# Kernel optimization log

Measured on AMD Instinct MI355X. Metric: run time of the kernel, lower is better.

## Reference

```python
import jax, jax.numpy as jnp
import numpy as np

N = 50000      # nodes
E = 800000     # edges (before self-loops)
IN_DIM = 128
OUT_DIM = 64   # per-head channels C (concat=False)
HEADS = 4
NEG_SLOPE = 0.2


def setup_inputs() -> dict:
    key = jax.random.key(0)
    ks = jax.random.split(key, 10)
    x = jax.random.normal(ks[0], (N, IN_DIM), dtype=jnp.float32)
    edge_index = jax.random.randint(ks[1], (2, E), 0, N, dtype=jnp.int32)
    # GAT parameters
    W = jax.random.normal(ks[2], (IN_DIM, HEADS * OUT_DIM), dtype=jnp.float32) * 0.05
    att_src = jax.random.normal(ks[3], (HEADS, OUT_DIM), dtype=jnp.float32) * 0.05
    att_dst = jax.random.normal(ks[4], (HEADS, OUT_DIM), dtype=jnp.float32) * 0.05
    bias = jnp.zeros((OUT_DIM,), dtype=jnp.float32)
    # LayerNorm + PReLU parameters
    gamma = jnp.ones((OUT_DIM,), dtype=jnp.float32)
    beta = jnp.zeros((OUT_DIM,), dtype=jnp.float32)
    prelu_w = jnp.full((1,), 0.25, dtype=jnp.float32)
    return {"x": x, "edge_index": edge_index, "W": W, "att_src": att_src,
            "att_dst": att_dst, "bias": bias, "gamma": gamma, "beta": beta,
            "prelu_w": prelu_w}


def reference(x, edge_index, W, att_src, att_dst, bias, gamma, beta, prelu_w):
    n = x.shape[0]
    # PyG GATConv default add_self_loops=True
    loops = jnp.arange(n, dtype=edge_index.dtype)
    src = jnp.concatenate([edge_index[0], loops])  # message sources j
    dst = jnp.concatenate([edge_index[1], loops])  # message targets i

    # linear projection into heads: [N, H, C]
    h = (x @ W).reshape(n, HEADS, OUT_DIM)
    a_src = jnp.einsum('nhc,hc->nh', h, att_src)  # [N, H]
    a_dst = jnp.einsum('nhc,hc->nh', h, att_dst)  # [N, H]

    # per-edge attention logits, leaky relu
    alpha = a_src[src] + a_dst[dst]                       # [E', H]
    alpha = jnp.where(alpha >= 0, alpha, NEG_SLOPE * alpha)

    # segment softmax over incoming edges of each destination node
    amax = jax.ops.segment_max(alpha, dst, num_segments=n)   # [N, H]
    e = jnp.exp(alpha - amax[dst])
    denom = jax.ops.segment_sum(e, dst, num_segments=n)      # [N, H]
    w = e / denom[dst]                                       # [E', H]

    # weighted scatter-aggregate of messages
    msg = h[src] * w[:, :, None]                             # [E', H, C]
    out = jax.ops.segment_sum(msg, dst, num_segments=n)      # [N, H, C]

    # concat=False -> mean over heads, then bias
    out = out.mean(axis=1) + bias                            # [N, C]

    # LayerNorm
    mu = out.mean(axis=-1, keepdims=True)
    var = out.var(axis=-1, keepdims=True)
    out = (out - mu) * jax.lax.rsqrt(var + 1e-5) * gamma + beta

    # PReLU (single shared weight)
    return jnp.where(out >= 0, out, prelu_w[0] * out)
```

## Files before the change

kernel.cpp:

```cpp
#include <hip/hip_runtime.h>

#define HEADS 4
#define CDIM  64
#define INDIM 128
#define NEG   0.2f
#define CAP     256
#define FASTCAP 252
#define NPB     256

typedef __attribute__((ext_vector_type(8))) short short8;
typedef __attribute__((ext_vector_type(4))) float f32x4;
typedef _Float16 half2_t __attribute__((ext_vector_type(2)));

__device__ __forceinline__ float wave_sum(float v) {
#pragma unroll
    for (int o = 32; o > 0; o >>= 1) v += __shfl_xor(v, o, 64);
    return v;
}
__device__ __forceinline__ int wave_sum_i(int v) {
#pragma unroll
    for (int o = 32; o > 0; o >>= 1) v += __shfl_xor(v, o, 64);
    return v;
}

__device__ __forceinline__ unsigned short f2bf(float f) {
    unsigned u = __float_as_uint(f);
    u = (u + 0x7FFFu + ((u >> 16) & 1u)) >> 16;
    return (unsigned short)u;
}

__device__ __forceinline__ unsigned pk_f16(float a, float b) {
    auto h = __builtin_amdgcn_cvt_pkrtz(a, b);
    return __builtin_bit_cast(unsigned, h);
}
__device__ __forceinline__ half2_t as_h2(unsigned u) {
    return __builtin_bit_cast(half2_t, u);
}

#if __has_builtin(__builtin_amdgcn_fdot2)
__device__ __forceinline__ float fdot2(unsigned a, unsigned b, float c) {
    return __builtin_amdgcn_fdot2(as_h2(a), as_h2(b), c, false);
}
#else
__device__ __forceinline__ float fdot2(unsigned a, unsigned b, float c) {
    half2_t ha = as_h2(a), hb = as_h2(b);
    return c + (float)ha.x * (float)hb.x + (float)ha.y * (float)hb.y;
}
#endif

__device__ __forceinline__ float lrelu(float a) { return a >= 0.f ? a : NEG * a; }

__global__ __launch_bounds__(256) void k_prep(const float* __restrict__ W,
    const float* __restrict__ att_src, const float* __restrict__ att_dst,
    unsigned short* __restrict__ Waug)
{
    const int wv = threadIdx.x >> 6, lane = threadIdx.x & 63;
    const int c = blockIdx.x * 4 + wv;
    if (c >= 272) return;
#pragma unroll
    for (int kk = 0; kk < 2; ++kk) {
        int k = lane + kk * 64;
        float val;
        if (c < 256) {
            val = W[k * 256 + c];
        } else if (c < 260) {
            int q = c - 256; float s = 0.f;
            for (int j = 0; j < 64; ++j) s += W[k * 256 + q * 64 + j] * att_src[q * 64 + j];
            val = s;
        } else if (c < 264) {
            int q = c - 260; float s = 0.f;
            for (int j = 0; j < 64; ++j) s += W[k * 256 + q * 64 + j] * att_dst[q * 64 + j];
            val = s;
        } else {
            val = 0.f;
        }
        Waug[c * 128 + k] = f2bf(val);
    }
}

__global__ __launch_bounds__(512) void gemm_mfma(
    const float* __restrict__ x, const unsigned short* __restrict__ Waug,
    uint2* __restrict__ hp, float* __restrict__ a_src, float* __restrict__ a_dst,
    int N)
{
    extern __shared__ char smem[];
    const int t = threadIdx.x;

    const uint4* srcw = (const uint4*)Waug;
    for (int i = t; i < 272 * 16; i += 512) {
        int col = i >> 4, kc = i & 15;
        int off = col * 256 + ((kc * 16) ^ ((col & 7) << 4));
        *(uint4*)(smem + off) = srcw[i];
    }
    __syncthreads();

    const int lane = t & 63, wv = t >> 6;
    const int l = lane & 15, g = lane >> 4;
    const int rowbase = blockIdx.x * 128 + wv * 16;

    int anode = rowbase + l; if (anode >= N) anode = N - 1;
    const float4* xrow = (const float4*)(x + (size_t)anode * INDIM);

    short8 af[4];
#pragma unroll
    for (int ks = 0; ks < 4; ++ks) {
        float4 x0 = xrow[ks * 8 + g * 2];
        float4 x1 = xrow[ks * 8 + g * 2 + 1];
        short8 a;
        a[0] = (short)f2bf(x0.x); a[1] = (short)f2bf(x0.y);
        a[2] = (short)f2bf(x0.z); a[3] = (short)f2bf(x0.w);
        a[4] = (short)f2bf(x1.x); a[5] = (short)f2bf(x1.y);
        a[6] = (short)f2bf(x1.z); a[7] = (short)f2bf(x1.w);
        af[ks] = a;
    }

    f32x4 acc[17];
    const f32x4 zero = {0.f, 0.f, 0.f, 0.f};
#pragma unroll
    for (int tt = 0; tt < 17; ++tt) acc[tt] = zero;

    const int base_b = l * 256;
#pragma unroll
    for (int ks = 0; ks < 4; ++ks) {
        const int koff = (ks * 64 + g * 16) ^ ((l & 7) << 4);
#pragma unroll
        for (int tt = 0; tt < 17; ++tt) {
            short8 bf = *(const short8*)(smem + tt * 4096 + base_b + koff);
            acc[tt] = __builtin_amdgcn_mfma_f32_16x16x32_bf16(af[ks], bf, acc[tt], 0, 0, 0);
        }
    }

#pragma unroll
    for (int j = 0; j < 4; ++j) {
        int node = rowbase + g * 4 + j;
        if (node < N) {
#pragma unroll
            for (int u = 0; u < 4; ++u) {
                int ch = l + 16 * u;
                hp[(size_t)node * CDIM + ch] = make_uint2(
                    pk_f16(acc[u][j],     acc[4 + u][j]),
                    pk_f16(acc[8 + u][j], acc[12 + u][j]));
            }
            if (l < 4)      a_src[node * 4 + l]       = acc[16][j];
            else if (l < 8) a_dst[node * 4 + (l - 4)] = acc[16][j];
        }
    }
}


__global__ __launch_bounds__(256) void k_count(const int* __restrict__ ei,
    int E, int EPB, int NBUK, int* __restrict__ counts)
{
    __shared__ int hist[256];
    const int t = threadIdx.x, blk = blockIdx.x;
    if (t < NBUK) hist[t] = 0;
    __syncthreads();
    const int e0 = blk * EPB;
    for (int j = t; j < EPB; j += 256) {
        int e = e0 + j;
        if (e < E) atomicAdd(&hist[ei[E + e] >> 8], 1);
    }
    __syncthreads();
    if (t < NBUK) counts[t * NPB + blk] = hist[t];
}

__global__ __launch_bounds__(256) void k_scan1(const int* __restrict__ arr,
    int* __restrict__ bsum, int n)
{
    const int t = threadIdx.x, lane = t & 63, wv = t >> 6;
    int gid = blockIdx.x * 256 + t;
    int v = (gid < n) ? arr[gid] : 0;
    v = wave_sum_i(v);
    __shared__ int ws[4];
    if (lane == 0) ws[wv] = v;
    __syncthreads();
    if (t == 0) bsum[blockIdx.x] = ws[0] + ws[1] + ws[2] + ws[3];
}

__global__ __launch_bounds__(1024) void k_scan2(int* __restrict__ bsum, int NB)
{
    __shared__ int lds[1024];
    const int t = threadIdx.x;
    int v = (t < NB) ? bsum[t] : 0;
    lds[t] = v;
    __syncthreads();
    for (int o = 1; o < 1024; o <<= 1) {
        int u = (t >= o) ? lds[t - o] : 0;
        __syncthreads();
        lds[t] += u;
        __syncthreads();
    }
    if (t < NB) bsum[t] = lds[t] - v;
}

__global__ __launch_bounds__(256) void k_scanip(int* __restrict__ arr,
    const int* __restrict__ bsum, int n)
{
    const int t = threadIdx.x, lane = t & 63, wv = t >> 6;
    int gid = blockIdx.x * 256 + t;
    int v = (gid < n) ? arr[gid] : 0;
    int inc = v;
#pragma unroll
    for (int o = 1; o < 64; o <<= 1) {
        int u = __shfl_up(inc, o, 64);
        if (lane >= o) inc += u;
    }
    __shared__ int wtot[4];
    if (lane == 63) wtot[wv] = inc;
    __syncthreads();
    int wpre = 0;
    for (int w = 0; w < wv; ++w) wpre += wtot[w];
    int ex = inc - v + wpre + bsum[blockIdx.x];
    if (gid < n) arr[gid] = ex;
}

__global__ __launch_bounds__(256) void k_part(const int* __restrict__ ei,
    int E, int EPB, int NBUK, const int* __restrict__ counts,
    uint2* __restrict__ srt)
{
    __shared__ int cb[256];
    const int t = threadIdx.x, blk = blockIdx.x;
    if (t < NBUK) cb[t] = counts[t * NPB + blk];
    __syncthreads();
    const int e0 = blk * EPB;
    for (int j = t; j < EPB; j += 256) {
        int e = e0 + j;
        if (e < E) {
            int s = ei[e], d = ei[E + e];
            int pos = atomicAdd(&cb[d >> 8], 1);
            srt[pos] = make_uint2((unsigned)s, (unsigned)d);
        }
    }
}

__global__ __launch_bounds__(256) void k_bcsr(const uint2* __restrict__ srt,
    const int* __restrict__ counts, int E, int N, int NBUK,
    int* __restrict__ deg, int* __restrict__ off, int* __restrict__ csr)
{
    __shared__ int h[256];
    __shared__ int cur[256];
    __shared__ int wt[4];
    const int t = threadIdx.x, b = blockIdx.x;
    const int bb0 = counts[b * NPB];
    const int bb1 = (b + 1 < NBUK) ? counts[(b + 1) * NPB] : E;
    const int ne = bb1 - bb0;

    h[t] = 0;
    __syncthreads();
    for (int j = t; j < ne; j += 256) atomicAdd(&h[srt[bb0 + j].y & 255], 1);
    __syncthreads();

    int v = h[t];
    const int lane = t & 63, wv = t >> 6;
    int inc = v;
#pragma unroll
    for (int o = 1; o < 64; o <<= 1) {
        int u = __shfl_up(inc, o, 64);
        if (lane >= o) inc += u;
    }
    if (lane == 63) wt[wv] = inc;
    __syncthreads();
    int wpre = 0;
    for (int w = 0; w < wv; ++w) wpre += wt[w];
    int ex = inc - v + wpre;

    int node = (b << 8) + t;
    if (node < N) { deg[node] = v; off[node] = bb0 + ex; }
    cur[t] = bb0 + ex;
    __syncthreads();

    for (int j = t; j < ne; j += 256) {
        uint2 u = srt[bb0 + j];
        int pos = atomicAdd(&cur[u.y & 255], 1);
        csr[pos] = (int)u.x;
    }
}

__global__ __launch_bounds__(256) void aggr_fused(
    const int* __restrict__ off, const int* __restrict__ deg,
    const int* __restrict__ csr_src,
    const float4* __restrict__ a_src4, const float4* __restrict__ a_dst4,
    const uint2* __restrict__ hp,
    const float* __restrict__ bias, const float* __restrict__ gamma,
    const float* __restrict__ beta, const float* __restrict__ prelu,
    float* __restrict__ out, int N)
{
    __shared__ uint4 slot[4][CAP];
    const int wv   = threadIdx.x >> 6;
    const int lane = threadIdx.x & 63;
    const int wid  = (int)(blockIdx.x * 4u + wv);
    if (wid >= N) return;
    const int d = wid;
    uint4* sl = slot[wv];

    const float4 ad = a_dst4[d];
    const int deg_d = deg[d];
    const int beg   = off[d];
    const int nv    = deg_d < FASTCAP ? deg_d : FASTCAP;
    const int nv4   = (nv + 3) & ~3;

    float dl0 = 0.f, dl1 = 0.f, dl2 = 0.f, dl3 = 0.f;
    for (int base = 0; base < deg_d; base += 64) {
        int j = base + lane;
        bool valid = j < deg_d;
        int sv = valid ? csr_src[beg + j] : 0;
        float4 as = a_src4[sv];
        float e0 = valid ? __expf(lrelu(as.x + ad.x)) : 0.f;
        float e1 = valid ? __expf(lrelu(as.y + ad.y)) : 0.f;
        float e2 = valid ? __expf(lrelu(as.z + ad.z)) : 0.f;
        float e3 = valid ? __expf(lrelu(as.w + ad.w)) : 0.f;
        dl0 += e0; dl1 += e1; dl2 += e2; dl3 += e3;
        if (j < CAP) sl[j] = make_uint4(pk_f16(e0, e1), pk_f16(e2, e3), (unsigned)sv, 0u);
    }

    float4 asd = a_src4[d];
    float es0 = __expf(lrelu(asd.x + ad.x));
    float es1 = __expf(lrelu(asd.y + ad.y));
    float es2 = __expf(lrelu(asd.z + ad.z));
    float es3 = __expf(lrelu(asd.w + ad.w));

    float r0 = __builtin_amdgcn_rcpf(wave_sum(dl0) + es0);
    float r1 = __builtin_amdgcn_rcpf(wave_sum(dl1) + es1);
    float r2 = __builtin_amdgcn_rcpf(wave_sum(dl2) + es2);
    float r3 = __builtin_amdgcn_rcpf(wave_sum(dl3) + es3);

    for (int base = 0; base < nv4; base += 64) {
        int j = base + lane;
        if (j < nv) {
            uint2 ev = *(const uint2*)&sl[j];
            half2_t e01 = as_h2(ev.x), e23 = as_h2(ev.y);
            *(uint2*)&sl[j] = make_uint2(
                pk_f16((float)e01.x * r0, (float)e01.y * r1),
                pk_f16((float)e23.x * r2, (float)e23.y * r3));
        } else if (j < nv4) {
            sl[j] = make_uint4(0u, 0u, 0u, 0u);
        }
    }
    __builtin_amdgcn_wave_barrier();

    uint2 hd = hp[(size_t)d * CDIM + lane];
    unsigned pw01 = pk_f16(es0 * r0, es1 * r1);
    unsigned pw23 = pk_f16(es2 * r2, es3 * r3);
    float acc01 = fdot2(pw01, hd.x, 0.f);
    float acc23 = fdot2(pw23, hd.y, 0.f);

    if (nv4 >= 8) {
        uint4 c0 = sl[0], c1 = sl[1], c2 = sl[2], c3 = sl[3];
        uint2 h0 = hp[(size_t)c0.z * CDIM + lane];
        uint2 h1 = hp[(size_t)c1.z * CDIM + lane];
        uint2 h2 = hp[(size_t)c2.z * CDIM + lane];
        uint2 h3 = hp[(size_t)c3.z * CDIM + lane];
        int j = 0;
        for (; j + 7 < nv4; j += 4) {
            uint4 n0 = sl[j + 4], n1 = sl[j + 5], n2 = sl[j + 6], n3 = sl[j + 7];
            uint2 g0 = hp[(size_t)n0.z * CDIM + lane];
            uint2 g1 = hp[(size_t)n1.z * CDIM + lane];
            uint2 g2 = hp[(size_t)n2.z * CDIM + lane];
            uint2 g3 = hp[(size_t)n3.z * CDIM + lane];
            acc01 = fdot2(c0.x, h0.x, acc01); acc23 = fdot2(c0.y, h0.y, acc23);
            acc01 = fdot2(c1.x, h1.x, acc01); acc23 = fdot2(c1.y, h1.y, acc23);
            acc01 = fdot2(c2.x, h2.x, acc01); acc23 = fdot2(c2.y, h2.y, acc23);
            acc01 = fdot2(c3.x, h3.x, acc01); acc23 = fdot2(c3.y, h3.y, acc23);
            c0 = n0; c1 = n1; c2 = n2; c3 = n3;
            h0 = g0; h1 = g1; h2 = g2; h3 = g3;
        }
        acc01 = fdot2(c0.x, h0.x, acc01); acc23 = fdot2(c0.y, h0.y, acc23);
        acc01 = fdot2(c1.x, h1.x, acc01); acc23 = fdot2(c1.y, h1.y, acc23);
        acc01 = fdot2(c2.x, h2.x, acc01); acc23 = fdot2(c2.y, h2.y, acc23);
        acc01 = fdot2(c3.x, h3.x, acc01); acc23 = fdot2(c3.y, h3.y, acc23);
    } else if (nv4 == 4) {
        uint4 c0 = sl[0], c1 = sl[1], c2 = sl[2], c3 = sl[3];
        uint2 h0 = hp[(size_t)c0.z * CDIM + lane];
        uint2 h1 = hp[(size_t)c1.z * CDIM + lane];
        uint2 h2 = hp[(size_t)c2.z * CDIM + lane];
        uint2 h3 = hp[(size_t)c3.z * CDIM + lane];
        acc01 = fdot2(c0.x, h0.x, acc01); acc23 = fdot2(c0.y, h0.y, acc23);
        acc01 = fdot2(c1.x, h1.x, acc01); acc23 = fdot2(c1.y, h1.y, acc23);
        acc01 = fdot2(c2.x, h2.x, acc01); acc23 = fdot2(c2.y, h2.y, acc23);
        acc01 = fdot2(c3.x, h3.x, acc01); acc23 = fdot2(c3.y, h3.y, acc23);
    }

    for (int base = FASTCAP; base < deg_d; base += 64) {
        int jj = base + lane;
        bool valid = jj < deg_d;
        int sv = valid ? csr_src[beg + jj] : 0;
        float4 as = a_src4[sv];
        float e0 = valid ? __expf(lrelu(as.x + ad.x)) : 0.f;
        float e1 = valid ? __expf(lrelu(as.y + ad.y)) : 0.f;
        float e2 = valid ? __expf(lrelu(as.z + ad.z)) : 0.f;
        float e3 = valid ? __expf(lrelu(as.w + ad.w)) : 0.f;
        sl[lane] = make_uint4(pk_f16(e0 * r0, e1 * r1), pk_f16(e2 * r2, e3 * r3),
                              (unsigned)sv, 0u);
        __builtin_amdgcn_wave_barrier();
        int nav = deg_d - base; if (nav > 64) nav = 64;
        for (int q = 0; q < nav; ++q) {
            uint4 t0 = sl[q];
            uint2 h0 = hp[(size_t)t0.z * CDIM + lane];
            acc01 = fdot2(t0.x, h0.x, acc01);
            acc23 = fdot2(t0.y, h0.y, acc23);
        }
        __builtin_amdgcn_wave_barrier();
    }

    float v = 0.25f * (acc01 + acc23) + bias[lane];
    float mu  = wave_sum(v) * (1.f / 64.f);
    float df  = v - mu;
    float var = wave_sum(df * df) * (1.f / 64.f);
    float rs  = rsqrtf(var + 1e-5f);
    float o   = df * rs * gamma[lane] + beta[lane];
    float pw  = prelu[0];
    o = o >= 0.f ? o : pw * o;
    out[(size_t)d * CDIM + lane] = o;
}

extern "C" void kernel_launch(void* const* d_in, const int* in_sizes, int n_in,
                              void* d_out, int out_size, void* d_ws, size_t ws_size,
                              hipStream_t stream)
{
    const float* x       = (const float*)d_in[0];
    const int*   ei      = (const int*)  d_in[1];
    const float* W       = (const float*)d_in[2];
    const float* att_src = (const float*)d_in[3];
    const float* att_dst = (const float*)d_in[4];
    const float* bias    = (const float*)d_in[5];
    const float* gamma   = (const float*)d_in[6];
    const float* beta    = (const float*)d_in[7];
    const float* prelu   = (const float*)d_in[8];

    const int N = in_sizes[0] / INDIM;
    const int E = in_sizes[1] / 2;
    float* out = (float*)d_out;

    const int NBUK = (N + 255) >> 8;
    const int EPB  = (E + NPB - 1) / NPB;
    const int NCNT = NBUK * NPB;

    uint2* hp     = (uint2*)d_ws;
    float* a_src  = (float*)(hp + (size_t)N * CDIM);
    float* a_dst  = a_src + (size_t)N * HEADS;
    int*   deg    = (int*)(a_dst + (size_t)N * HEADS);
    int*   off    = deg + N;
    int*   counts = off + N;
    int*   bsum   = counts + NCNT;
    uint2* srt    = (uint2*)(bsum + 1024);
    int*   csr    = (int*)(srt + E);
    unsigned short* Waug = (unsigned short*)(csr + E);

    k_prep<<<68, 256, 0, stream>>>(W, att_src, att_dst, Waug);

    k_count<<<NPB, 256, 0, stream>>>(ei, E, EPB, NBUK, counts);
    k_scan1<<<NBUK, 256, 0, stream>>>(counts, bsum, NCNT);
    k_scan2<<<1, 1024, 0, stream>>>(bsum, NBUK);
    k_scanip<<<NBUK, 256, 0, stream>>>(counts, bsum, NCNT);
    k_part<<<NPB, 256, 0, stream>>>(ei, E, EPB, NBUK, counts, srt);
    k_bcsr<<<NBUK, 256, 0, stream>>>(srt, counts, E, N, NBUK, deg, off, csr);

    gemm_mfma<<<(N + 127) / 128, 512, 69632, stream>>>(
        x, Waug, hp, a_src, a_dst, N);

    aggr_fused<<<(N + 3) / 4, 256, 0, stream>>>(
        off, deg, csr, (const float4*)a_src, (const float4*)a_dst, hp,
        bias, gamma, beta, prelu, out, N);
}
```

Measured before the change: 119.6 us.

## Merge prep into count kernel, fold scan passes, pack sorted edges into 32 bits

The weight-prep kernel is merged into the edge-histogram kernel, and the standalone block-sum scan is removed: each scan block now reduces the preceding block sums itself. Together this drops two kernel launches from the CSR build pipeline. The partitioned edge buffer is packed as (src<<8 | dst&255) in one 32-bit word instead of a uint2, halving traffic in the partition and bucket-CSR passes. This assumes src fits in 24 bits, which holds for N=50000. The aggregation epilogue also hoists the bias, gamma, beta and prelu loads to the kernel start.

```diff
diff --git a/kernel.cpp b/kernel.cpp
--- a/kernel.cpp
+++ b/kernel.cpp
@@ -50,16 +50,26 @@
 
 __device__ __forceinline__ float lrelu(float a) { return a >= 0.f ? a : NEG * a; }
 
-__global__ __launch_bounds__(256) void k_prep(const float* __restrict__ W,
-    const float* __restrict__ att_src, const float* __restrict__ att_dst,
-    unsigned short* __restrict__ Waug)
-{
-    const int wv = threadIdx.x >> 6, lane = threadIdx.x & 63;
-    const int c = blockIdx.x * 4 + wv;
-    if (c >= 272) return;
-#pragma unroll
-    for (int kk = 0; kk < 2; ++kk) {
-        int k = lane + kk * 64;
+__global__ __launch_bounds__(256) void k_count_prep(const int* __restrict__ ei,
+    int E, int EPB, int NBUK, int* __restrict__ counts,
+    const float* __restrict__ W, const float* __restrict__ att_src,
+    const float* __restrict__ att_dst, unsigned short* __restrict__ Waug)
+{
+    __shared__ int hist[256];
+    const int t = threadIdx.x, blk = blockIdx.x;
+    hist[t] = 0;
+    __syncthreads();
+    const int e0 = blk * EPB;
+    for (int j = t; j < EPB; j += 256) {
+        int e = e0 + j;
+        if (e < E) atomicAdd(&hist[ei[E + e] >> 8], 1);
+    }
+    __syncthreads();
+    if (t < NBUK) counts[t * NPB + blk] = hist[t];
+
+    int idx = blk * 256 + t;
+    if (idx < 272 * 128) {
+        int c = idx >> 7, k = idx & 127;
         float val;
         if (c < 256) {
             val = W[k * 256 + c];
@@ -78,6 +88,112 @@
     }
 }
 
+__global__ __launch_bounds__(256) void k_scan1(const int* __restrict__ arr,
+    int* __restrict__ bsum, int n)
+{
+    const int t = threadIdx.x, lane = t & 63, wv = t >> 6;
+    int gid = blockIdx.x * 256 + t;
+    int v = (gid < n) ? arr[gid] : 0;
+    v = wave_sum_i(v);
+    __shared__ int ws[4];
+    if (lane == 0) ws[wv] = v;
+    __syncthreads();
+    if (t == 0) bsum[blockIdx.x] = ws[0] + ws[1] + ws[2] + ws[3];
+}
+
+__global__ __launch_bounds__(256) void k_scanip2(int* __restrict__ arr,
+    const int* __restrict__ bsum, int NB, int n)
+{
+    __shared__ int wred[4];
+    __shared__ int wtot[4];
+    __shared__ int spre;
+    const int t = threadIdx.x, lane = t & 63, wv = t >> 6, b = blockIdx.x;
+
+    int u0 = (t < NB && t < b) ? bsum[t] : 0;
+    u0 = wave_sum_i(u0);
+    if (lane == 0) wred[wv] = u0;
+    __syncthreads();
+    if (t == 0) spre = wred[0] + wred[1] + wred[2] + wred[3];
+    __syncthreads();
+
+    int gid = b * 256 + t;
+    int v = (gid < n) ? arr[gid] : 0;
+    int inc = v;
+#pragma unroll
+    for (int o = 1; o < 64; o <<= 1) {
+        int u = __shfl_up(inc, o, 64);
+        if (lane >= o) inc += u;
+    }
+    if (lane == 63) wtot[wv] = inc;
+    __syncthreads();
+    int wpre = 0;
+    for (int w = 0; w < wv; ++w) wpre += wtot[w];
+    int ex = inc - v + wpre + spre;
+    if (gid < n) arr[gid] = ex;
+}
+
+__global__ __launch_bounds__(256) void k_part(const int* __restrict__ ei,
+    int E, int EPB, int NBUK, const int* __restrict__ counts,
+    unsigned* __restrict__ srt)
+{
+    __shared__ int cb[256];
+    const int t = threadIdx.x, blk = blockIdx.x;
+    if (t < NBUK) cb[t] = counts[t * NPB + blk];
+    __syncthreads();
+    const int e0 = blk * EPB;
+    for (int j = t; j < EPB; j += 256) {
+        int e = e0 + j;
+        if (e < E) {
+            int s = ei[e], d = ei[E + e];
+            int pos = atomicAdd(&cb[d >> 8], 1);
+            srt[pos] = ((unsigned)s << 8) | ((unsigned)d & 255u);
+        }
+    }
+}
+
+__global__ __launch_bounds__(256) void k_bcsr(const unsigned* __restrict__ srt,
+    const int* __restrict__ counts, int E, int N, int NBUK,
+    int* __restrict__ deg, int* __restrict__ off, int* __restrict__ csr)
+{
+    __shared__ int h[256];
+    __shared__ int cur[256];
+    __shared__ int wt[4];
+    const int t = threadIdx.x, b = blockIdx.x;
+    const int bb0 = counts[b * NPB];
+    const int bb1 = (b + 1 < NBUK) ? counts[(b + 1) * NPB] : E;
+    const int ne = bb1 - bb0;
+
+    h[t] = 0;
+    __syncthreads();
+    for (int j = t; j < ne; j += 256) atomicAdd(&h[srt[bb0 + j] & 255u], 1);
+    __syncthreads();
+
+    int v = h[t];
+    const int lane = t & 63, wv = t >> 6;
+    int inc = v;
+#pragma unroll
+    for (int o = 1; o < 64; o <<= 1) {
+        int u = __shfl_up(inc, o, 64);
+        if (lane >= o) inc += u;
+    }
+    if (lane == 63) wt[wv] = inc;
+    __syncthreads();
+    int wpre = 0;
+    for (int w = 0; w < wv; ++w) wpre += wt[w];
+    int ex = inc - v + wpre;
+
+    int node = (b << 8) + t;
+    if (node < N) { deg[node] = v; off[node] = bb0 + ex; }
+    cur[t] = bb0 + ex;
+    __syncthreads();
+
+    for (int j = t; j < ne; j += 256) {
+        unsigned u = srt[bb0 + j];
+        int pos = atomicAdd(&cur[u & 255u], 1);
+        csr[pos] = (int)(u >> 8);
+    }
+}
+
 __global__ __launch_bounds__(512) void gemm_mfma(
     const float* __restrict__ x, const unsigned short* __restrict__ Waug,
     uint2* __restrict__ hp, float* __restrict__ a_src, float* __restrict__ a_dst,
@@ -147,135 +263,6 @@
     }
 }
 
-
-__global__ __launch_bounds__(256) void k_count(const int* __restrict__ ei,
-    int E, int EPB, int NBUK, int* __restrict__ counts)
-{
-    __shared__ int hist[256];
-    const int t = threadIdx.x, blk = blockIdx.x;
-    if (t < NBUK) hist[t] = 0;
-    __syncthreads();
-    const int e0 = blk * EPB;
-    for (int j = t; j < EPB; j += 256) {
-        int e = e0 + j;
-        if (e < E) atomicAdd(&hist[ei[E + e] >> 8], 1);
-    }
-    __syncthreads();
-    if (t < NBUK) counts[t * NPB + blk] = hist[t];
-}
-
-__global__ __launch_bounds__(256) void k_scan1(const int* __restrict__ arr,
-    int* __restrict__ bsum, int n)
-{
-    const int t = threadIdx.x, lane = t & 63, wv = t >> 6;
-    int gid = blockIdx.x * 256 + t;
-    int v = (gid < n) ? arr[gid] : 0;
-    v = wave_sum_i(v);
-    __shared__ int ws[4];
-    if (lane == 0) ws[wv] = v;
-    __syncthreads();
-    if (t == 0) bsum[blockIdx.x] = ws[0] + ws[1] + ws[2] + ws[3];
-}
-
-__global__ __launch_bounds__(1024) void k_scan2(int* __restrict__ bsum, int NB)
-{
-    __shared__ int lds[1024];
-    const int t = threadIdx.x;
-    int v = (t < NB) ? bsum[t] : 0;
-    lds[t] = v;
-    __syncthreads();
-    for (int o = 1; o < 1024; o <<= 1) {
-        int u = (t >= o) ? lds[t - o] : 0;
-        __syncthreads();
-        lds[t] += u;
-        __syncthreads();
-    }
-    if (t < NB) bsum[t] = lds[t] - v;
-}
-
-__global__ __launch_bounds__(256) void k_scanip(int* __restrict__ arr,
-    const int* __restrict__ bsum, int n)
-{
-    const int t = threadIdx.x, lane = t & 63, wv = t >> 6;
-    int gid = blockIdx.x * 256 + t;
-    int v = (gid < n) ? arr[gid] : 0;
-    int inc = v;
-#pragma unroll
-    for (int o = 1; o < 64; o <<= 1) {
-        int u = __shfl_up(inc, o, 64);
-        if (lane >= o) inc += u;
-    }
-    __shared__ int wtot[4];
-    if (lane == 63) wtot[wv] = inc;
-    __syncthreads();
-    int wpre = 0;
-    for (int w = 0; w < wv; ++w) wpre += wtot[w];
-    int ex = inc - v + wpre + bsum[blockIdx.x];
-    if (gid < n) arr[gid] = ex;
-}
-
-__global__ __launch_bounds__(256) void k_part(const int* __restrict__ ei,
-    int E, int EPB, int NBUK, const int* __restrict__ counts,
-    uint2* __restrict__ srt)
-{
-    __shared__ int cb[256];
-    const int t = threadIdx.x, blk = blockIdx.x;
-    if (t < NBUK) cb[t] = counts[t * NPB + blk];
-    __syncthreads();
-    const int e0 = blk * EPB;
-    for (int j = t; j < EPB; j += 256) {
-        int e = e0 + j;
-        if (e < E) {
-            int s = ei[e], d = ei[E + e];
-            int pos = atomicAdd(&cb[d >> 8], 1);
-            srt[pos] = make_uint2((unsigned)s, (unsigned)d);
-        }
-    }
-}
-
-__global__ __launch_bounds__(256) void k_bcsr(const uint2* __restrict__ srt,
-    const int* __restrict__ counts, int E, int N, int NBUK,
-    int* __restrict__ deg, int* __restrict__ off, int* __restrict__ csr)
-{
-    __shared__ int h[256];
-    __shared__ int cur[256];
-    __shared__ int wt[4];
-    const int t = threadIdx.x, b = blockIdx.x;
-    const int bb0 = counts[b * NPB];
-    const int bb1 = (b + 1 < NBUK) ? counts[(b + 1) * NPB] : E;
-    const int ne = bb1 - bb0;
-
-    h[t] = 0;
-    __syncthreads();
-    for (int j = t; j < ne; j += 256) atomicAdd(&h[srt[bb0 + j].y & 255], 1);
-    __syncthreads();
-
-    int v = h[t];
-    const int lane = t & 63, wv = t >> 6;
-    int inc = v;
-#pragma unroll
-    for (int o = 1; o < 64; o <<= 1) {
-        int u = __shfl_up(inc, o, 64);
-        if (lane >= o) inc += u;
-    }
-    if (lane == 63) wt[wv] = inc;
-    __syncthreads();
-    int wpre = 0;
-    for (int w = 0; w < wv; ++w) wpre += wt[w];
-    int ex = inc - v + wpre;
-
-    int node = (b << 8) + t;
-    if (node < N) { deg[node] = v; off[node] = bb0 + ex; }
-    cur[t] = bb0 + ex;
-    __syncthreads();
-
-    for (int j = t; j < ne; j += 256) {
-        uint2 u = srt[bb0 + j];
-        int pos = atomicAdd(&cur[u.y & 255], 1);
-        csr[pos] = (int)u.x;
-    }
-}
-
 __global__ __launch_bounds__(256) void aggr_fused(
     const int* __restrict__ off, const int* __restrict__ deg,
     const int* __restrict__ csr_src,
@@ -293,6 +280,7 @@
     const int d = wid;
     uint4* sl = slot[wv];
 
+    const float bl = bias[lane], gl = gamma[lane], bt = beta[lane], pw = prelu[0];
     const float4 ad = a_dst4[d];
     const int deg_d = deg[d];
     const int beg   = off[d];
@@ -402,13 +390,12 @@
         __builtin_amdgcn_wave_barrier();
     }
 
-    float v = 0.25f * (acc01 + acc23) + bias[lane];
+    float v = 0.25f * (acc01 + acc23) + bl;
     float mu  = wave_sum(v) * (1.f / 64.f);
     float df  = v - mu;
     float var = wave_sum(df * df) * (1.f / 64.f);
     float rs  = rsqrtf(var + 1e-5f);
-    float o   = df * rs * gamma[lane] + beta[lane];
-    float pw  = prelu[0];
+    float o   = df * rs * gl + bt;
     o = o >= 0.f ? o : pw * o;
     out[(size_t)d * CDIM + lane] = o;
 }
@@ -435,23 +422,21 @@
     const int EPB  = (E + NPB - 1) / NPB;
     const int NCNT = NBUK * NPB;
 
-    uint2* hp     = (uint2*)d_ws;
-    float* a_src  = (float*)(hp + (size_t)N * CDIM);
-    float* a_dst  = a_src + (size_t)N * HEADS;
-    int*   deg    = (int*)(a_dst + (size_t)N * HEADS);
-    int*   off    = deg + N;
-    int*   counts = off + N;
-    int*   bsum   = counts + NCNT;
-    uint2* srt    = (uint2*)(bsum + 1024);
-    int*   csr    = (int*)(srt + E);
+    uint2*    hp     = (uint2*)d_ws;
+    float*    a_src  = (float*)(hp + (size_t)N * CDIM);
+    float*    a_dst  = a_src + (size_t)N * HEADS;
+    int*      deg    = (int*)(a_dst + (size_t)N * HEADS);
+    int*      off    = deg + N;
+    int*      counts = off + N;
+    int*      bsum   = counts + NCNT;
+    unsigned* srt    = (unsigned*)(bsum + 1024);
+    int*      csr    = (int*)(srt + E);
     unsigned short* Waug = (unsigned short*)(csr + E);
 
-    k_prep<<<68, 256, 0, stream>>>(W, att_src, att_dst, Waug);
-
-    k_count<<<NPB, 256, 0, stream>>>(ei, E, EPB, NBUK, counts);
+    k_count_prep<<<NPB, 256, 0, stream>>>(ei, E, EPB, NBUK, counts,
+                                          W, att_src, att_dst, Waug);
     k_scan1<<<NBUK, 256, 0, stream>>>(counts, bsum, NCNT);
-    k_scan2<<<1, 1024, 0, stream>>>(bsum, NBUK);
-    k_scanip<<<NBUK, 256, 0, stream>>>(counts, bsum, NCNT);
+    k_scanip2<<<NBUK, 256, 0, stream>>>(counts, bsum, NBUK, NCNT);
     k_part<<<NPB, 256, 0, stream>>>(ei, E, EPB, NBUK, counts, srt);
     k_bcsr<<<NBUK, 256, 0, stream>>>(srt, counts, E, N, NBUK, deg, off, csr);
 
```

After: 115.7 us. 3.2% less time.
